# Optimization experiments

Hardware: AMD Instinct MI355X
Metric: run time of the kernel (lower is better)

Reference implementation:

```python
import jax, jax.numpy as jnp
import numpy as np
import math

SCALES = (128.0, 256.0, 512.0)
RATIOS = (0.5, 1.0, 2.0)
NMS_THR = 0.7
PRENMS_TOPK = 6000
POSTNMS_TOPK = 300
LOG_MAX = math.log(1000.0 / 16)  # clamp on dw/dh, as in torch code


def conv2d(x, w, b, pad):
    y = jax.lax.conv_general_dilated(x, w, (1, 1), [(pad, pad), (pad, pad)],
                                     dimension_numbers=('NCHW', 'OIHW', 'NCHW'))
    return y + b[None, :, None, None]


def generate_anchors(img_h, img_w, feat_h, feat_w):
    stride_h = img_h // feat_h
    stride_w = img_w // feat_w
    base = []
    for s in SCALES:
        for r in RATIOS:
            w = s * math.sqrt(1.0 / r)
            h = s * math.sqrt(r)
            base.append([-w / 2, -h / 2, w / 2, h / 2])
    base = jnp.asarray(base, jnp.float32)  # [A,4]
    sx = jnp.arange(feat_w, dtype=jnp.float32) * stride_w + stride_w // 2
    sy = jnp.arange(feat_h, dtype=jnp.float32) * stride_h + stride_h // 2
    syy, sxx = jnp.meshgrid(sy, sx, indexing='ij')
    sxf = sxx.reshape(-1)
    syf = syy.reshape(-1)
    shifts = jnp.stack([sxf, syf, sxf, syf], axis=1)  # [HW,4]
    anchors = (shifts[:, None, :] + base[None, :, :]).reshape(-1, 4)  # [HW*A,4]
    return anchors


def decode(reg, anchors):
    # reg, anchors: [N,4]
    w = anchors[:, 2] - anchors[:, 0]
    h = anchors[:, 3] - anchors[:, 1]
    cx = anchors[:, 0] + 0.5 * w
    cy = anchors[:, 1] + 0.5 * h
    dx, dy = reg[:, 0], reg[:, 1]
    dw = jnp.minimum(reg[:, 2], LOG_MAX)
    dh = jnp.minimum(reg[:, 3], LOG_MAX)
    pcx = dx * w + cx
    pcy = dy * h + cy
    pw = jnp.exp(dw) * w
    ph = jnp.exp(dh) * h
    return jnp.stack([pcx - 0.5 * pw, pcy - 0.5 * ph,
                      pcx + 0.5 * pw, pcy + 0.5 * ph], axis=1)


def nms_fixed(boxes, scores, thr, k):
    # Greedy NMS, fixed k iterations; suppressed/invalid entries have score -inf.
    x1, y1, x2, y2 = boxes[:, 0], boxes[:, 1], boxes[:, 2], boxes[:, 3]
    areas = (x2 - x1) * (y2 - y1)

    def step(live, _):
        best = jnp.argmax(live)
        ok = live[best] > -jnp.inf
        b = boxes[best]
        xl = jnp.maximum(b[0], x1)
        yt = jnp.maximum(b[1], y1)
        xr = jnp.minimum(b[2], x2)
        yb = jnp.minimum(b[3], y2)
        inter = jnp.clip(xr - xl, 0.0) * jnp.clip(yb - yt, 0.0)
        iou = inter / (areas[best] + areas - inter)
        live = jnp.where(iou > thr, -jnp.inf, live).at[best].set(-jnp.inf)
        return live, (best.astype(jnp.int32), ok)

    _, (keep, valid) = jax.lax.scan(step, scores, None, length=k)
    return keep, valid


def setup_inputs() -> dict:
    key = jax.random.key(0)
    ks = jax.random.split(key, 6)
    C = 512
    A = len(SCALES) * len(RATIOS)
    return {
        'image': jax.random.normal(ks[0], (8, 3, 1024, 1024), jnp.float32),
        'feat': jax.random.normal(ks[1], (8, C, 64, 64), jnp.float32),
        'conv_w': jax.random.normal(ks[2], (C, C, 3, 3), jnp.float32) * 0.01,
        'conv_b': jnp.zeros((C,), jnp.float32),
        'cls_w': jax.random.normal(ks[3], (A, C, 1, 1), jnp.float32) * 0.01,
        'cls_b': jnp.zeros((A,), jnp.float32),
        'reg_w': jax.random.normal(ks[4], (4 * A, C, 1, 1), jnp.float32) * 0.01,
        'reg_b': jnp.zeros((4 * A,), jnp.float32),
    }


def reference(image, feat, conv_w, conv_b, cls_w, cls_b, reg_w, reg_b):
    t = jax.nn.relu(conv2d(feat, conv_w, conv_b, 1))
    cls = conv2d(t, cls_w, cls_b, 0)   # [B,A,H,W]
    reg = conv2d(t, reg_w, reg_b, 0)   # [B,4A,H,W]
    B, _, H, W = cls.shape
    img_h, img_w = image.shape[-2], image.shape[-1]
    anchors = generate_anchors(img_h, img_w, H, W)  # [H*W*A,4]

    cls0 = cls[0].transpose(1, 2, 0).reshape(-1)        # permute(0,2,3,1): H,W,A order
    reg0 = reg[0].transpose(1, 2, 0).reshape(-1, 4)
    proposals = decode(reg0, anchors)
    scores = jax.nn.sigmoid(jax.lax.stop_gradient(cls0))  # cls_scores.detach()

    k = min(PRENMS_TOPK, scores.shape[0])
    top_scores, top_idx = jax.lax.top_k(scores, k)
    props = proposals[top_idx]
    props = jnp.stack([jnp.clip(props[:, 0], 0.0, float(img_w)),
                       jnp.clip(props[:, 1], 0.0, float(img_h)),
                       jnp.clip(props[:, 2], 0.0, float(img_w)),
                       jnp.clip(props[:, 3], 0.0, float(img_h))], axis=1)
    wv = props[:, 2] - props[:, 0]
    hv = props[:, 3] - props[:, 1]
    valid = (wv >= 1.0) & (hv >= 1.0)   # tiny boxes masked out instead of filtered
    sc = jnp.where(valid, top_scores, -jnp.inf)

    keep, kvalid = nms_fixed(jax.lax.stop_gradient(props), sc, NMS_THR, POSTNMS_TOPK)
    out_boxes = jnp.where(kvalid[:, None], props[keep], 0.0)   # [300,4]
    out_scores = jnp.where(kvalid, top_scores[keep], 0.0)      # [300]
    return jnp.concatenate([out_boxes, out_scores[:, None]], axis=1)  # [300,5]
```

## Files before the change

kernel.cpp:

```cpp
#include <hip/hip_runtime.h>
#include <math.h>

#define NMS_THRESH 0.7f
#define NANCH 36864
#define TOPK 6000
#define NWORDS 94
#define POSTK 300
#define MAXCAND 10240

__global__ __launch_bounds__(256, 2)
void k_conv(const float* __restrict__ feat, const float* __restrict__ W,
            const float* __restrict__ bias, float* __restrict__ tout)
{
    __shared__ float sF[16 * 6 * 68];
    __shared__ float sW[16 * 10 * 16];

    const int blk = blockIdx.x;
    const int ct  = blk & 31;
    const int yt  = blk >> 5;
    const int cob = ct << 4;
    const int y0  = yt << 2;
    const int tid = threadIdx.x;
    const int lane = tid & 63;
    const int wid = __builtin_amdgcn_readfirstlane(tid >> 6);
    const int co0 = cob + (wid << 2);
    const int cwo = wid << 2;
    const int ly = lane >> 4;
    const int lx = (lane & 15) << 2;

    int g_ofs[7]; int l_ofs[7]; bool g_ok[7]; bool w_do[7];
    #pragma unroll
    for (int q = 0; q < 7; ++q) {
        int u = q * 256 + tid;
        int ci = u / 102; int rem = u - ci * 102;
        int rr = rem / 17; int seg = rem - rr * 17;
        int gy = y0 - 1 + rr;
        w_do[q] = (u < 1632);
        g_ok[q] = w_do[q] && (seg < 16) && (gy >= 0) && (gy < 64);
        g_ofs[q] = ((ci & 15) << 12) + ((gy & 63) << 6) + ((seg & 15) << 2);
        l_ofs[q] = ci * 408 + rr * 68 + (seg << 2);
    }

    const int sci = tid >> 4, sco = tid & 15;
    const float* wsrc = W + (size_t)(cob + sco) * 4608 + sci * 9;

    float acc[4][4];
    #pragma unroll
    for (int i = 0; i < 4; ++i)
        #pragma unroll
        for (int j = 0; j < 4; ++j) acc[i][j] = 0.f;

    for (int cc = 0; cc < 32; ++cc) {
        __syncthreads();
        {
            const float* fsrc = feat + ((size_t)cc << 16);
            float4 r[7];
            #pragma unroll
            for (int q = 0; q < 7; ++q)
                r[q] = g_ok[q] ? *(const float4*)(fsrc + g_ofs[q])
                               : make_float4(0.f, 0.f, 0.f, 0.f);
            #pragma unroll
            for (int q = 0; q < 7; ++q)
                if (w_do[q]) *(float4*)&sF[l_ofs[q]] = r[q];
        }
        {
            const float* wp = wsrc + (size_t)cc * 144;
            float wv[9];
            #pragma unroll
            for (int t = 0; t < 9; ++t) wv[t] = wp[t];
            #pragma unroll
            for (int t = 0; t < 9; ++t)
                sW[sci * 160 + t * 16 + sco] = wv[t];
        }
        __syncthreads();
        #pragma unroll 2
        for (int ci = 0; ci < 16; ++ci) {
            #pragma unroll
            for (int ky = 0; ky < 3; ++ky) {
                const float* rb = sF + ci * 408 + (ly + ky) * 68;
                float4 f4 = *(const float4*)&rb[lx];
                int c0 = lx ? lx - 1 : 0;
                int c5 = (lx < 60) ? lx + 4 : 63;
                float t0 = rb[c0];
                float t5 = rb[c5];
                float fr[6];
                fr[0] = lx ? t0 : 0.f;
                fr[1] = f4.x; fr[2] = f4.y; fr[3] = f4.z; fr[4] = f4.w;
                fr[5] = (lx < 60) ? t5 : 0.f;
                const float* wb = sW + ci * 160 + (ky * 3) * 16 + cwo;
                float w_[3][4];
                *(float4*)w_[0] = *(const float4*)(wb);
                *(float4*)w_[1] = *(const float4*)(wb + 16);
                *(float4*)w_[2] = *(const float4*)(wb + 32);
                #pragma unroll
                for (int kx = 0; kx < 3; ++kx)
                    #pragma unroll
                    for (int i = 0; i < 4; ++i)
                        #pragma unroll
                        for (int j = 0; j < 4; ++j)
                            acc[i][j] = fmaf(fr[i + kx], w_[kx][j], acc[i][j]);
            }
        }
    }

    const int y = y0 + ly;
    #pragma unroll
    for (int j = 0; j < 4; ++j) {
        const float bv = bias[co0 + j];
        float4 o;
        o.x = fmaxf(acc[0][j] + bv, 0.f);
        o.y = fmaxf(acc[1][j] + bv, 0.f);
        o.z = fmaxf(acc[2][j] + bv, 0.f);
        o.w = fmaxf(acc[3][j] + bv, 0.f);
        *(float4*)&tout[((size_t)(co0 + j) << 12) + (y << 6) + lx] = o;
    }
}

__global__ __launch_bounds__(64)
void k_heads(const float* __restrict__ t, const float* __restrict__ cls_w,
             const float* __restrict__ cls_b, const float* __restrict__ reg_w,
             const float* __restrict__ reg_b, float* __restrict__ heads)
{
    const int bid = blockIdx.x;
    const int ch = bid % 45;
    const int pt = bid / 45;
    const int px = (pt << 6) + threadIdx.x;
    const float* wp; float bv;
    if (ch < 9) { wp = cls_w + ch * 512;       bv = cls_b[ch]; }
    else        { wp = reg_w + (ch - 9) * 512; bv = reg_b[ch - 9]; }
    float acc = bv;
    #pragma unroll 8
    for (int ci = 0; ci < 512; ++ci)
        acc = fmaf(t[((size_t)ci << 12) + px], wp[ci], acc);
    heads[((size_t)ch << 12) + px] = acc;
}

__global__ void k_decode(const float* __restrict__ heads,
                         float* __restrict__ score, float* __restrict__ validf,
                         float* __restrict__ box, unsigned* __restrict__ hist)
{
    __shared__ unsigned lh[4096];
    const int tid = threadIdx.x;
    for (int q = tid; q < 4096; q += 256) lh[q] = 0u;
    __syncthreads();

    int idx = blockIdx.x * 256 + tid;
    int p = idx / 9, a = idx - p * 9;
    int yq = p >> 6, xq = p & 63;
    const double scl[3] = {128.0, 256.0, 512.0};
    const double rat[3] = {0.5, 1.0, 2.0};
    double s = scl[a / 3], r = rat[a % 3];
    float bw = (float)(s * sqrt(1.0 / r) * 0.5);
    float bh = (float)(s * sqrt(r) * 0.5);
    float sx = xq * 16.0f + 8.0f;
    float sy = yq * 16.0f + 8.0f;
    float a0 = sx - bw, a1 = sy - bh, a2 = sx + bw, a3 = sy + bh;
    float wa = a2 - a0, ha = a3 - a1;
    float cx = a0 + 0.5f * wa, cy = a1 + 0.5f * ha;
    float logit = heads[(size_t)a * 4096 + p];
    float dx = heads[(size_t)(9  + 4 * a) * 4096 + p];
    float dy = heads[(size_t)(10 + 4 * a) * 4096 + p];
    float dw = fminf(heads[(size_t)(11 + 4 * a) * 4096 + p], 4.135166556742356f);
    float dh = fminf(heads[(size_t)(12 + 4 * a) * 4096 + p], 4.135166556742356f);
    float pcx = dx * wa + cx, pcy = dy * ha + cy;
    float pw = expf(dw) * wa, ph = expf(dh) * ha;
    float x1 = pcx - 0.5f * pw, y1 = pcy - 0.5f * ph;
    float x2 = pcx + 0.5f * pw, y2 = pcy + 0.5f * ph;
    x1 = fminf(fmaxf(x1, 0.f), 1024.f); y1 = fminf(fmaxf(y1, 0.f), 1024.f);
    x2 = fminf(fmaxf(x2, 0.f), 1024.f); y2 = fminf(fmaxf(y2, 0.f), 1024.f);
    float wv = x2 - x1, hv = y2 - y1;
    float sc = 1.f / (1.f + expf(-logit));
    score[idx]  = sc;
    validf[idx] = (wv >= 1.f && hv >= 1.f) ? 1.f : 0.f;
    box[idx * 4 + 0] = x1; box[idx * 4 + 1] = y1;
    box[idx * 4 + 2] = x2; box[idx * 4 + 3] = y2;

    atomicAdd(&lh[__float_as_uint(sc) >> 19], 1u);
    __syncthreads();
    for (int q = tid; q < 4096; q += 256) if (lh[q]) atomicAdd(&hist[q], lh[q]);
}

__global__ void k_zero(unsigned* __restrict__ p) {
    int i = blockIdx.x * 256 + threadIdx.x;
    if (i < 8448) p[i] = 0u;
}

__global__ void k_cut1(const unsigned* __restrict__ hist, unsigned* __restrict__ meta) {
    __shared__ unsigned hh[4096];
    __shared__ unsigned gs[256];
    int tid = threadIdx.x;
    for (int q = tid; q < 4096; q += 256) hh[q] = hist[q];
    __syncthreads();
    unsigned s = 0;
    #pragma unroll
    for (int k = 0; k < 16; ++k) s += hh[tid * 16 + k];
    gs[tid] = s;
    __syncthreads();
    if (tid == 0) {
        unsigned cum = 0;
        for (int g = 255; g >= 0; --g) {
            if (cum + gs[g] >= (unsigned)TOPK) {
                for (int b = g * 16 + 15; b >= g * 16; --b) {
                    if (cum + hh[b] >= (unsigned)TOPK) { meta[2] = (unsigned)b; meta[3] = cum; break; }
                    cum += hh[b];
                }
                break;
            }
            cum += gs[g];
        }
    }
}

__global__ void k_hist2(const float* __restrict__ score, const unsigned* __restrict__ meta,
                        unsigned* __restrict__ hist2) {
    int idx = blockIdx.x * 256 + threadIdx.x;
    unsigned bits = __float_as_uint(score[idx]);
    if ((bits >> 19) == meta[2]) atomicAdd(&hist2[(bits >> 7) & 0xFFFu], 1u);
}

__global__ void k_cut2(const unsigned* __restrict__ hist2, unsigned* __restrict__ meta) {
    __shared__ unsigned hh[4096];
    __shared__ unsigned gs[256];
    int tid = threadIdx.x;
    for (int q = tid; q < 4096; q += 256) hh[q] = hist2[q];
    __syncthreads();
    unsigned s = 0;
    #pragma unroll
    for (int k = 0; k < 16; ++k) s += hh[tid * 16 + k];
    gs[tid] = s;
    __syncthreads();
    if (tid == 0) {
        unsigned cum = meta[3];
        unsigned B = meta[2];
        unsigned cut = B << 19;
        for (int g = 255; g >= 0; --g) {
            if (cum + gs[g] >= (unsigned)TOPK) {
                for (int b = g * 16 + 15; b >= g * 16; --b) {
                    cum += hh[b];
                    if (cum >= (unsigned)TOPK) { cut = (B << 19) | ((unsigned)b << 7); break; }
                }
                break;
            }
            cum += gs[g];
        }
        meta[0] = cut;
    }
}

__global__ void k_compact(const float* __restrict__ score, unsigned* __restrict__ meta,
                          int* __restrict__ cand, float* __restrict__ cscore) {
    int idx = blockIdx.x * 256 + threadIdx.x;
    unsigned bits = __float_as_uint(score[idx]);
    if (bits >= meta[0]) {
        unsigned pos = atomicAdd(&meta[1], 1u);
        if (pos < (unsigned)MAXCAND) {
            cand[pos] = idx;
            cscore[pos] = __uint_as_float(bits);
        }
    }
}

__global__ __launch_bounds__(256, 4)
void k_rank(const float* __restrict__ score, const float* __restrict__ validf,
            const float* __restrict__ box, const unsigned* __restrict__ meta,
            const int* __restrict__ cand, const float* __restrict__ cscore,
            float* __restrict__ score6, float* __restrict__ sc6,
            float* __restrict__ box6)
{
    __shared__ int pc[8][32];
    const int tid = threadIdx.x;
    const int il = tid & 31, js = tid >> 5;
    unsigned ncand = meta[1]; if (ncand > (unsigned)MAXCAND) ncand = MAXCAND;
    const int c = blockIdx.x * 32 + il;
    int i = -1; float si = 0.f;
    if (c < (int)ncand) { i = cand[c]; si = cscore[c]; }
    int cnt = 0;
    {
        const float4* cs4 = (const float4*)cscore;
        const int4*   cd4 = (const int4*)cand;
        const int q0 = js * 320;
        for (int q = 0; q < 320; ++q) {
            float4 v = cs4[q0 + q];
            int4   w = cd4[q0 + q];
            cnt += (v.x > si) || (v.x == si && w.x < i);
            cnt += (v.y > si) || (v.y == si && w.y < i);
            cnt += (v.z > si) || (v.z == si && w.z < i);
            cnt += (v.w > si) || (v.w == si && w.w < i);
        }
    }
    pc[js][il] = cnt;
    __syncthreads();
    if (js == 0 && i >= 0) {
        int rank = 0;
        #pragma unroll
        for (int q = 0; q < 8; ++q) rank += pc[q][il];
        if (rank < TOPK) {
            score6[rank] = si;
            sc6[rank] = (validf[i] != 0.f) ? si : -INFINITY;
            box6[rank * 4 + 0] = box[i * 4 + 0];
            box6[rank * 4 + 1] = box[i * 4 + 1];
            box6[rank * 4 + 2] = box[i * 4 + 2];
            box6[rank * 4 + 3] = box[i * 4 + 3];
        }
    }
}

__global__ void k_iou(const float* __restrict__ box6,
                      unsigned long long* __restrict__ mask)
{
    __shared__ float jb[64][4];
    const int blk = blockIdx.x;
    const int rb = blk / NWORDS, wb = blk - rb * NWORDS;
    const int tid = threadIdx.x;
    int j = wb * 64 + tid;
    if (j < TOPK) {
        jb[tid][0] = box6[j * 4 + 0]; jb[tid][1] = box6[j * 4 + 1];
        jb[tid][2] = box6[j * 4 + 2]; jb[tid][3] = box6[j * 4 + 3];
    } else {
        jb[tid][0] = 0.f; jb[tid][1] = 0.f; jb[tid][2] = 0.f; jb[tid][3] = 0.f;
    }
    __syncthreads();
    int i = rb * 64 + tid;
    if (i >= TOPK) return;
    float x1 = box6[i * 4], y1 = box6[i * 4 + 1], x2 = box6[i * 4 + 2], y2 = box6[i * 4 + 3];
    float ai = (x2 - x1) * (y2 - y1);
    unsigned long long bits = 0;
    for (int q = 0; q < 64; ++q) {
        float bx1 = jb[q][0], by1 = jb[q][1], bx2 = jb[q][2], by2 = jb[q][3];
        float xl = fmaxf(x1, bx1), yt = fmaxf(y1, by1);
        float xr = fminf(x2, bx2), yb = fminf(y2, by2);
        float inter = fmaxf(xr - xl, 0.f) * fmaxf(yb - yt, 0.f);
        float aj = (bx2 - bx1) * (by2 - by1);
        float iou = inter / (ai + aj - inter);
        if (iou > NMS_THRESH) bits |= (1ull << q);
    }
    mask[(size_t)i * NWORDS + wb] = bits;
}

__global__ void k_scan(const float* __restrict__ sc6, const float* __restrict__ score6,
                       const float* __restrict__ box6,
                       const unsigned long long* __restrict__ mask,
                       float* __restrict__ out)
{
    __shared__ unsigned long long remv[NWORDS];
    __shared__ int kept[POSTK];
    __shared__ int kcnt;
    __shared__ int kbs_s;
    __shared__ int klist[64];
    const int tid = threadIdx.x;
    for (int w = tid; w < NWORDS; w += 256) remv[w] = 0ull;
    if (tid == 0) kcnt = 0;
    __syncthreads();
    for (int b = 0; b < NWORDS; ++b) {
        if (tid < 64) {
            int i = b * 64 + tid;
            bool v = (i < TOPK) && (sc6[i] > -INFINITY);
            unsigned long long mi = 0ull;
            if (v) mi = mask[(size_t)i * NWORDS + b];
            unsigned long long validb = __ballot(v);
            unsigned long long cur = remv[b];
            int kc = kcnt;
            int kb = 0;
            unsigned long long cand2 = validb & ~cur;
            while (cand2 != 0ull && kc < POSTK) {
                int rr = __builtin_ctzll(cand2);
                unsigned long long mr = __shfl(mi, rr, 64);
                if (tid == 0) { kept[kc] = b * 64 + rr; klist[kb] = rr; }
                ++kb; ++kc;
                cur |= mr | (1ull << rr);
                cand2 = validb & ~cur;
            }
            if (tid == 0) { kcnt = kc; kbs_s = kb; remv[b] = cur; }
        }
        __syncthreads();
        int kb = kbs_s;
        if (kb > 0) {
            int w = b + 1 + tid;
            if (w < NWORDS) {
                unsigned long long acc = remv[w];
                for (int q = 0; q < kb; ++q) {
                    int rr = klist[q];
                    acc |= mask[(size_t)(b * 64 + rr) * NWORDS + w];
                }
                remv[w] = acc;
            }
        }
        __syncthreads();
        if (kcnt >= POSTK) break;
    }
    __syncthreads();
    int kc = kcnt;
    for (int n = tid; n < POSTK; n += 256) {
        float o0 = 0.f, o1 = 0.f, o2 = 0.f, o3 = 0.f, o4 = 0.f;
        if (n < kc) {
            int i = kept[n];
            o0 = box6[i * 4 + 0]; o1 = box6[i * 4 + 1];
            o2 = box6[i * 4 + 2]; o3 = box6[i * 4 + 3];
            o4 = score6[i];
        }
        out[n * 5 + 0] = o0; out[n * 5 + 1] = o1; out[n * 5 + 2] = o2;
        out[n * 5 + 3] = o3; out[n * 5 + 4] = o4;
    }
}

extern "C" void kernel_launch(void* const* d_in, const int* in_sizes, int n_in,
                              void* d_out, int out_size, void* d_ws, size_t ws_size,
                              hipStream_t stream)
{
    (void)in_sizes; (void)n_in; (void)out_size; (void)ws_size;
    const float* feat   = (const float*)d_in[1];
    const float* conv_w = (const float*)d_in[2];
    const float* conv_b = (const float*)d_in[3];
    const float* cls_w  = (const float*)d_in[4];
    const float* cls_b  = (const float*)d_in[5];
    const float* reg_w  = (const float*)d_in[6];
    const float* reg_b  = (const float*)d_in[7];

    char* ws = (char*)d_ws;
    float*    t      = (float*)(ws + 0);
    float*    heads  = (float*)(ws + 8388608);
    unsigned* hist   = (unsigned*)(ws + 9125888);
    unsigned* hist2  = (unsigned*)(ws + 9142272);
    unsigned* meta   = (unsigned*)(ws + 9158656);
    int*      cand   = (int*)(ws + 9158720);
    float*    cscore = (float*)(ws + 9199680);
    float*    score  = (float*)(ws + 9240640);
    float*    validf = (float*)(ws + 9388096);
    float*    box    = (float*)(ws + 9535552);
    float*    score6 = (float*)(ws + 10125376);
    float*    sc6    = (float*)(ws + 10149952);
    float*    box6   = (float*)(ws + 10174528);
    unsigned long long* mask = (unsigned long long*)(ws + 0);

    k_zero   <<<33,   256, 0, stream>>>(hist);
    k_conv   <<<512,  256, 0, stream>>>(feat, conv_w, conv_b, t);
    k_heads  <<<2880, 64,  0, stream>>>(t, cls_w, cls_b, reg_w, reg_b, heads);
    k_decode <<<144,  256, 0, stream>>>(heads, score, validf, box, hist);
    k_cut1   <<<1,    256, 0, stream>>>(hist, meta);
    k_hist2  <<<144,  256, 0, stream>>>(score, meta, hist2);
    k_cut2   <<<1,    256, 0, stream>>>(hist2, meta);
    k_compact<<<144,  256, 0, stream>>>(score, meta, cand, cscore);
    k_rank   <<<320,  256, 0, stream>>>(score, validf, box, meta, cand, cscore, score6, sc6, box6);
    k_iou    <<<NWORDS * NWORDS, 64, 0, stream>>>(box6, mask);
    k_scan   <<<1,    256, 0, stream>>>(sc6, score6, box6, mask, (float*)d_out);
}
```

Before: 534.2 us.

## Double-buffer conv shared-memory tiles and replace IoU-mask NMS with on-the-fly single-block NMS

The conv kernel now double-buffers the feature tile in shared memory and prefetches the next channel chunk's features and weights into registers while computing the current chunk. This hides global load latency behind the FMA loop, at the cost of about 52KB of shared memory per block, which may reduce occupancy. Separately, the full 6000x6000 IoU bitmask kernel and the scan are replaced by one 512-thread block. That block tests each 64-box batch against the boxes already kept, with 8 waves splitting the kept list. This drops a large mask write and read, but serialises all IoU work in one block.

```diff
diff --git a/kernel.cpp b/kernel.cpp
--- a/kernel.cpp
+++ b/kernel.cpp
@@ -12,7 +12,7 @@
 void k_conv(const float* __restrict__ feat, const float* __restrict__ W,
             const float* __restrict__ bias, float* __restrict__ tout)
 {
-    __shared__ float sF[16 * 6 * 68];
+    __shared__ float sF[2 * 6528];
     __shared__ float sW[16 * 10 * 16];
 
     const int blk = blockIdx.x;
@@ -50,34 +50,44 @@
         #pragma unroll
         for (int j = 0; j < 4; ++j) acc[i][j] = 0.f;
 
+    float wreg[9];
+    {
+        float4 r0[7];
+        #pragma unroll
+        for (int q = 0; q < 7; ++q)
+            r0[q] = g_ok[q] ? *(const float4*)(feat + g_ofs[q])
+                            : make_float4(0.f, 0.f, 0.f, 0.f);
+        #pragma unroll
+        for (int q = 0; q < 7; ++q)
+            if (w_do[q]) *(float4*)&sF[l_ofs[q]] = r0[q];
+        #pragma unroll
+        for (int t = 0; t < 9; ++t) wreg[t] = wsrc[t];
+    }
+
+    int p = 0;
     for (int cc = 0; cc < 32; ++cc) {
-        __syncthreads();
-        {
-            const float* fsrc = feat + ((size_t)cc << 16);
-            float4 r[7];
+        const bool more = cc < 31;
+        #pragma unroll
+        for (int t = 0; t < 9; ++t)
+            sW[sci * 160 + t * 16 + sco] = wreg[t];
+        float4 r[7]; float wregN[9];
+        if (more) {
+            const float* fsrc = feat + ((size_t)(cc + 1) << 16);
             #pragma unroll
             for (int q = 0; q < 7; ++q)
                 r[q] = g_ok[q] ? *(const float4*)(fsrc + g_ofs[q])
                                : make_float4(0.f, 0.f, 0.f, 0.f);
+            const float* wp = wsrc + (size_t)(cc + 1) * 144;
             #pragma unroll
-            for (int q = 0; q < 7; ++q)
-                if (w_do[q]) *(float4*)&sF[l_ofs[q]] = r[q];
-        }
-        {
-            const float* wp = wsrc + (size_t)cc * 144;
-            float wv[9];
-            #pragma unroll
-            for (int t = 0; t < 9; ++t) wv[t] = wp[t];
-            #pragma unroll
-            for (int t = 0; t < 9; ++t)
-                sW[sci * 160 + t * 16 + sco] = wv[t];
+            for (int t = 0; t < 9; ++t) wregN[t] = wp[t];
         }
         __syncthreads();
+        const int pbase = p * 6528;
         #pragma unroll 2
         for (int ci = 0; ci < 16; ++ci) {
             #pragma unroll
             for (int ky = 0; ky < 3; ++ky) {
-                const float* rb = sF + ci * 408 + (ly + ky) * 68;
+                const float* rb = sF + pbase + ci * 408 + (ly + ky) * 68;
                 float4 f4 = *(const float4*)&rb[lx];
                 int c0 = lx ? lx - 1 : 0;
                 int c5 = (lx < 60) ? lx + 4 : 63;
@@ -101,6 +111,16 @@
                             acc[i][j] = fmaf(fr[i + kx], w_[kx][j], acc[i][j]);
             }
         }
+        if (more) {
+            const int wb2 = (p ^ 1) * 6528;
+            #pragma unroll
+            for (int q = 0; q < 7; ++q)
+                if (w_do[q]) *(float4*)&sF[wb2 + l_ofs[q]] = r[q];
+            #pragma unroll
+            for (int t = 0; t < 9; ++t) wreg[t] = wregN[t];
+        }
+        __syncthreads();
+        p ^= 1;
     }
 
     const int y = y0 + ly;
@@ -305,95 +325,81 @@
     }
 }
 
-__global__ void k_iou(const float* __restrict__ box6,
-                      unsigned long long* __restrict__ mask)
-{
-    __shared__ float jb[64][4];
-    const int blk = blockIdx.x;
-    const int rb = blk / NWORDS, wb = blk - rb * NWORDS;
-    const int tid = threadIdx.x;
-    int j = wb * 64 + tid;
-    if (j < TOPK) {
-        jb[tid][0] = box6[j * 4 + 0]; jb[tid][1] = box6[j * 4 + 1];
-        jb[tid][2] = box6[j * 4 + 2]; jb[tid][3] = box6[j * 4 + 3];
-    } else {
-        jb[tid][0] = 0.f; jb[tid][1] = 0.f; jb[tid][2] = 0.f; jb[tid][3] = 0.f;
-    }
-    __syncthreads();
-    int i = rb * 64 + tid;
-    if (i >= TOPK) return;
-    float x1 = box6[i * 4], y1 = box6[i * 4 + 1], x2 = box6[i * 4 + 2], y2 = box6[i * 4 + 3];
-    float ai = (x2 - x1) * (y2 - y1);
-    unsigned long long bits = 0;
-    for (int q = 0; q < 64; ++q) {
-        float bx1 = jb[q][0], by1 = jb[q][1], bx2 = jb[q][2], by2 = jb[q][3];
-        float xl = fmaxf(x1, bx1), yt = fmaxf(y1, by1);
-        float xr = fminf(x2, bx2), yb = fminf(y2, by2);
-        float inter = fmaxf(xr - xl, 0.f) * fmaxf(yb - yt, 0.f);
-        float aj = (bx2 - bx1) * (by2 - by1);
-        float iou = inter / (ai + aj - inter);
-        if (iou > NMS_THRESH) bits |= (1ull << q);
-    }
-    mask[(size_t)i * NWORDS + wb] = bits;
-}
-
-__global__ void k_scan(const float* __restrict__ sc6, const float* __restrict__ score6,
-                       const float* __restrict__ box6,
-                       const unsigned long long* __restrict__ mask,
-                       float* __restrict__ out)
-{
-    __shared__ unsigned long long remv[NWORDS];
-    __shared__ int kept[POSTK];
-    __shared__ int kcnt;
-    __shared__ int kbs_s;
-    __shared__ int klist[64];
-    const int tid = threadIdx.x;
-    for (int w = tid; w < NWORDS; w += 256) remv[w] = 0ull;
-    if (tid == 0) kcnt = 0;
-    __syncthreads();
+__global__ __launch_bounds__(512)
+void k_nms(const float* __restrict__ sc6, const float* __restrict__ score6,
+           const float* __restrict__ box6, float* __restrict__ out)
+{
+    __shared__ float kx1[POSTK], ky1[POSTK], kx2[POSTK], ky2[POSTK], kar[POSTK];
+    __shared__ int kidx[POSTK];
+    __shared__ unsigned long long pOR[8];
+    __shared__ int kcnt_s;
+    const int tid = threadIdx.x, lane = tid & 63, wv = tid >> 6;
+
+    if (tid == 0) kcnt_s = 0;
+    int i0 = lane;
+    float cx1 = box6[i0 * 4 + 0], cy1 = box6[i0 * 4 + 1];
+    float cx2 = box6[i0 * 4 + 2], cy2 = box6[i0 * 4 + 3];
+    float csc = sc6[i0];
+    __syncthreads();
+
     for (int b = 0; b < NWORDS; ++b) {
-        if (tid < 64) {
-            int i = b * 64 + tid;
-            bool v = (i < TOPK) && (sc6[i] > -INFINITY);
-            unsigned long long mi = 0ull;
-            if (v) mi = mask[(size_t)i * NWORDS + b];
+        float nx1 = 0.f, ny1 = 0.f, nx2 = 0.f, ny2 = 0.f, nsc = -INFINITY;
+        if (b + 1 < NWORDS) {
+            int ni = (b + 1) * 64 + lane; if (ni >= TOPK) ni = TOPK - 1;
+            nx1 = box6[ni * 4 + 0]; ny1 = box6[ni * 4 + 1];
+            nx2 = box6[ni * 4 + 2]; ny2 = box6[ni * 4 + 3];
+            nsc = sc6[ni];
+        }
+        const int i = b * 64 + lane;
+        const bool v = (i < TOPK) && (csc > -INFINITY);
+        const float ar = (cx2 - cx1) * (cy2 - cy1);
+        const int kc = kcnt_s;
+        bool dead = false;
+        for (int j = wv; j < kc; j += 8) {
+            float xl = fmaxf(kx1[j], cx1), yt = fmaxf(ky1[j], cy1);
+            float xr = fminf(kx2[j], cx2), yb = fminf(ky2[j], cy2);
+            float inter = fmaxf(xr - xl, 0.f) * fmaxf(yb - yt, 0.f);
+            float iou = inter / (kar[j] + ar - inter);
+            dead = dead || (iou > NMS_THRESH);
+        }
+        pOR[wv] = __ballot(dead);
+        __syncthreads();
+        if (wv == 0) {
+            unsigned long long supp = pOR[0] | pOR[1] | pOR[2] | pOR[3]
+                                    | pOR[4] | pOR[5] | pOR[6] | pOR[7];
             unsigned long long validb = __ballot(v);
-            unsigned long long cur = remv[b];
-            int kc = kcnt;
-            int kb = 0;
-            unsigned long long cand2 = validb & ~cur;
-            while (cand2 != 0ull && kc < POSTK) {
+            unsigned long long cand2 = validb & ~supp;
+            int kc2 = kc;
+            while (cand2 != 0ull && kc2 < POSTK) {
                 int rr = __builtin_ctzll(cand2);
-                unsigned long long mr = __shfl(mi, rr, 64);
-                if (tid == 0) { kept[kc] = b * 64 + rr; klist[kb] = rr; }
-                ++kb; ++kc;
-                cur |= mr | (1ull << rr);
-                cand2 = validb & ~cur;
+                float rx1 = __shfl(cx1, rr, 64), ry1 = __shfl(cy1, rr, 64);
+                float rx2 = __shfl(cx2, rr, 64), ry2 = __shfl(cy2, rr, 64);
+                float rar = __shfl(ar, rr, 64);
+                if (lane == 0) {
+                    kx1[kc2] = rx1; ky1[kc2] = ry1;
+                    kx2[kc2] = rx2; ky2[kc2] = ry2;
+                    kar[kc2] = rar; kidx[kc2] = b * 64 + rr;
+                }
+                float xl = fmaxf(rx1, cx1), yt = fmaxf(ry1, cy1);
+                float xr = fminf(rx2, cx2), yb = fminf(ry2, cy2);
+                float inter = fmaxf(xr - xl, 0.f) * fmaxf(yb - yt, 0.f);
+                float iou = inter / (rar + ar - inter);
+                unsigned long long sm = __ballot(iou > NMS_THRESH) | (1ull << rr);
+                cand2 &= ~sm;
+                ++kc2;
             }
-            if (tid == 0) { kcnt = kc; kbs_s = kb; remv[b] = cur; }
+            if (lane == 0) kcnt_s = kc2;
         }
         __syncthreads();
-        int kb = kbs_s;
-        if (kb > 0) {
-            int w = b + 1 + tid;
-            if (w < NWORDS) {
-                unsigned long long acc = remv[w];
-                for (int q = 0; q < kb; ++q) {
-                    int rr = klist[q];
-                    acc |= mask[(size_t)(b * 64 + rr) * NWORDS + w];
-                }
-                remv[w] = acc;
-            }
-        }
-        __syncthreads();
-        if (kcnt >= POSTK) break;
-    }
-    __syncthreads();
-    int kc = kcnt;
-    for (int n = tid; n < POSTK; n += 256) {
+        if (kcnt_s >= POSTK) break;
+        cx1 = nx1; cy1 = ny1; cx2 = nx2; cy2 = ny2; csc = nsc;
+    }
+
+    const int kc = kcnt_s;
+    for (int n = tid; n < POSTK; n += 512) {
         float o0 = 0.f, o1 = 0.f, o2 = 0.f, o3 = 0.f, o4 = 0.f;
         if (n < kc) {
-            int i = kept[n];
+            int i = kidx[n];
             o0 = box6[i * 4 + 0]; o1 = box6[i * 4 + 1];
             o2 = box6[i * 4 + 2]; o3 = box6[i * 4 + 3];
             o4 = score6[i];
@@ -430,7 +436,6 @@
     float*    score6 = (float*)(ws + 10125376);
     float*    sc6    = (float*)(ws + 10149952);
     float*    box6   = (float*)(ws + 10174528);
-    unsigned long long* mask = (unsigned long long*)(ws + 0);
 
     k_zero   <<<33,   256, 0, stream>>>(hist);
     k_conv   <<<512,  256, 0, stream>>>(feat, conv_w, conv_b, t);
@@ -441,6 +446,5 @@
     k_cut2   <<<1,    256, 0, stream>>>(hist2, meta);
     k_compact<<<144,  256, 0, stream>>>(score, meta, cand, cscore);
     k_rank   <<<320,  256, 0, stream>>>(score, validf, box, meta, cand, cscore, score6, sc6, box6);
-    k_iou    <<<NWORDS * NWORDS, 64, 0, stream>>>(box6, mask);
-    k_scan   <<<1,    256, 0, stream>>>(sc6, score6, box6, mask, (float*)d_out);
-}
+    k_nms    <<<1,    512, 0, stream>>>(sc6, score6, box6, (float*)d_out);
+}
```

Measured after the change: 520.7 us. -2.5%, faster.
